# Optimization experiments

Hardware: AMD Instinct MI355X
Metric: run time of the kernel (lower is better)

Reference implementation:

```python
import jax, jax.numpy as jnp
import numpy as np
from jax import lax

# ---- static config (from init_kwargs / input_specs) ----
B, NB, C, F = 16, 8192, 3, 64   # batches, points-per-batch, coord dim, feat dim
RATIO, K = 0.125, 16
M = int(RATIO * NB)


def setup_inputs() -> dict:
    key = jax.random.key(0)
    kx, kp = jax.random.split(key)
    x = jax.random.normal(kx, (B * NB, F), dtype=jnp.float32)
    pos = jax.random.normal(kp, (B * NB, C), dtype=jnp.float32)
    batch = (jnp.arange(B * NB, dtype=jnp.int32) // NB).astype(jnp.int32)
    return {"x": x, "pos": pos, "batch": batch}


def _fps_single(pos_b):
    """Sequential farthest point sampling on (NB, C), deterministic start at 0.
    Returns (M,) int32 indices into pos_b."""
    n = pos_b.shape[0]

    def step(carry, _):
        min_d2, last = carry
        d2 = jnp.sum((pos_b - pos_b[last]) ** 2, axis=-1)   # (NB,)
        min_d2 = jnp.minimum(min_d2, d2)
        nxt = jnp.argmax(min_d2).astype(jnp.int32)
        return (min_d2, nxt), last

    init = (jnp.full((n,), jnp.finfo(pos_b.dtype).max, dtype=pos_b.dtype),
            jnp.int32(0))
    _, idx = lax.scan(step, init, None, length=M)
    return idx  # (M,)


def reference(x, pos, batch):
    # batch ids are block-constant (batch[i] = i // NB), so per-batch views are
    # simple reshapes -- same semantics as torch_cluster's batched fps/knn.
    pos_b = pos.reshape(B, NB, C)

    # --- farthest point sampling per batch ---
    fps_idx = jax.vmap(_fps_single)(pos_b)                            # (B, M)
    centroids = jnp.take_along_axis(pos_b, fps_idx[..., None], axis=1)  # (B, M, C)

    # --- k-NN: squared distances centroids -> all points of same batch ---
    d2 = (jnp.sum(centroids ** 2, axis=-1)[..., None]
          - 2.0 * jnp.einsum('bmc,bnc->bmn', centroids, pos_b)
          + jnp.sum(pos_b ** 2, axis=-1)[:, None, :])                 # (B, M, NB)
    _, nn_idx = lax.top_k(-d2, K)                                     # (B, M, K)

    # gather neighbor coordinates (== pos[groups_idx[1]])
    groups = jax.vmap(lambda p, i: p[i])(pos_b, nn_idx.reshape(B, M * K))  # (B, M*K, C)

    return centroids.reshape(B * M, C), groups.reshape(B * M * K, C)
```

## Files before the change

kernel.cpp:

```cpp
#include <hip/hip_runtime.h>
#include <float.h>
#include <math.h>

#define B_   16
#define NB_  8192
#define M_   1024
#define K_   16


typedef float v2f __attribute__((ext_vector_type(2)));

#define FPS_T 256
#define PPT   32
#define NPAIR (PPT/2)
#define NWAVE (FPS_T/64)

__global__ __launch_bounds__(FPS_T, 1) void fps_kernel(const float* __restrict__ pos,
                                                       float* __restrict__ cent)
{
    #pragma clang fp contract(off)
    const int b = blockIdx.x;
    const int t = threadIdx.x;
    const float* pb = pos + (size_t)b * NB_ * 3;
    float* cb = cent + (size_t)b * M_ * 3;

    __shared__ float4 spts[NB_];
    __shared__ unsigned long long wkey[2][NWAVE];

    for (int p = t; p < NB_; p += FPS_T) {
        const float* s = pb + (size_t)p * 3;
        spts[p] = make_float4(s[0], s[1], s[2], 0.0f);
    }

    v2f px2[NPAIR], py2[NPAIR], pz2[NPAIR], md2[NPAIR];
    #pragma unroll
    for (int jj = 0; jj < NPAIR; ++jj) {
        const float* s0 = pb + (size_t)(t*PPT + 2*jj) * 3;
        px2[jj] = (v2f){s0[0], s0[3]};
        py2[jj] = (v2f){s0[1], s0[4]};
        pz2[jj] = (v2f){s0[2], s0[5]};
        md2[jj] = (v2f){FLT_MAX, FLT_MAX};
    }
    __syncthreads();

    float lx = pb[0], ly = pb[1], lz = pb[2];
    float c0x=0,c0y=0,c0z=0,c1x=0,c1y=0,c1z=0,c2x=0,c2y=0,c2z=0,c3x=0,c3y=0,c3z=0;

    for (int m = 0; m < M_; ++m) {
        if (t == (m >> 2)) {
            const int sl = m & 3;
            if      (sl == 0) { c0x=lx; c0y=ly; c0z=lz; }
            else if (sl == 1) { c1x=lx; c1y=ly; c1z=lz; }
            else if (sl == 2) { c2x=lx; c2y=ly; c2z=lz; }
            else              { c3x=lx; c3y=ly; c3z=lz; }
        }
        if (m == M_ - 1) break;

        const v2f lxv = {lx,lx}, lyv = {ly,ly}, lzv = {lz,lz};
        v2f bmax2 = {-1.0f, -1.0f};
        #pragma unroll
        for (int jj = 0; jj < NPAIR; ++jj) {
            v2f dx = px2[jj] - lxv;
            v2f dy = py2[jj] - lyv;
            v2f dz = pz2[jj] - lzv;
            v2f d2 = (dx*dx + dy*dy) + dz*dz;
            v2f mj = __builtin_elementwise_min(md2[jj], d2);
            md2[jj] = mj;
            bmax2 = __builtin_elementwise_max(bmax2, mj);
        }
        float bm = fmaxf(bmax2.x, bmax2.y);

        float v = bm;
        {
            int vi;
            vi = __builtin_amdgcn_update_dpp(__float_as_int(v), __float_as_int(v), 0xB1,  0xF, 0xF, false);
            v = fmaxf(v, __int_as_float(vi));
            vi = __builtin_amdgcn_update_dpp(__float_as_int(v), __float_as_int(v), 0x4E,  0xF, 0xF, false);
            v = fmaxf(v, __int_as_float(vi));
            vi = __builtin_amdgcn_update_dpp(__float_as_int(v), __float_as_int(v), 0x141, 0xF, 0xF, false);
            v = fmaxf(v, __int_as_float(vi));
            vi = __builtin_amdgcn_update_dpp(__float_as_int(v), __float_as_int(v), 0x140, 0xF, 0xF, false);
            v = fmaxf(v, __int_as_float(vi));
            vi = __builtin_amdgcn_update_dpp(__float_as_int(v), __float_as_int(v), 0x142, 0xF, 0xF, false);
            v = fmaxf(v, __int_as_float(vi));
            vi = __builtin_amdgcn_update_dpp(__float_as_int(v), __float_as_int(v), 0x143, 0xF, 0xF, false);
            v = fmaxf(v, __int_as_float(vi));
        }
        const float wv = __int_as_float(__builtin_amdgcn_readlane(__float_as_int(v), 63));

        int jp = -1;
        #pragma unroll
        for (int jj = NPAIR - 1; jj >= 0; --jj) {
            if (md2[jj].y == wv) jp = 2*jj + 1;
            if (md2[jj].x == wv) jp = 2*jj;
        }
        const unsigned long long mk = __ballot(jp >= 0);
        const int wl = (int)__ffsll(mk) - 1;
        const int gi = __builtin_amdgcn_readlane(t*PPT + jp, wl);

        const int par = m & 1;
        if ((t & 63) == 0)
            wkey[par][t >> 6] = ((unsigned long long)__float_as_uint(wv) << 32) |
                                (unsigned int)(~gi);
        __syncthreads();

        unsigned long long kk = wkey[par][0];
        #pragma unroll
        for (int w = 1; w < NWAVE; ++w) {
            const unsigned long long e = wkey[par][w];
            kk = (e > kk) ? e : kk;
        }
        const int best = (int)(~(unsigned int)kk);

        const float4 c = spts[best];
        lx = c.x; ly = c.y; lz = c.z;
    }

    {
        float4* o = (float4*)(cb + (size_t)t * 12);
        o[0] = make_float4(c0x, c0y, c0z, c1x);
        o[1] = make_float4(c1y, c1z, c2x, c2y);
        o[2] = make_float4(c2z, c3x, c3y, c3z);
    }
}

#define KNN_T   256
#define CHUNK   1024
#define GRP     8
#define BCAP    16
#define BSTRIDE 17

__device__ __forceinline__ void topk_insert(float d2, int pi, float val[16], int idx[16])
{
    int r = 0;
    #pragma unroll
    for (int j = 0; j < 16; ++j) r += (val[j] <= d2) ? 1 : 0;
    #pragma unroll
    for (int j = 15; j >= 1; --j) {
        bool sh = (j > r);
        val[j] = sh ? val[j-1] : val[j];
        idx[j] = sh ? idx[j-1] : idx[j];
    }
    #pragma unroll
    for (int j = 0; j < 16; ++j) {
        bool pl = (j == r);
        val[j] = pl ? d2 : val[j];
        idx[j] = pl ? pi : idx[j];
    }
}

__global__ __launch_bounds__(KNN_T, 2) void knn_kernel(const float* __restrict__ pos,
    const float* __restrict__ cent, float* __restrict__ groups,
    unsigned long long* __restrict__ partials, int nsplit)
{
    #pragma clang fp contract(off)
    __shared__ float4 spts[CHUNK];
    __shared__ unsigned long long sbuf[KNN_T * BSTRIDE];

    const int wg = blockIdx.x;
    const int t  = threadIdx.x;
    const int per_b = 4 * nsplit;
    const int b  = wg / per_b;
    const int r  = wg % per_b;
    const int cg = r / nsplit;
    const int sp = r % nsplit;
    const int span  = NB_ / nsplit;
    const int pbase = sp * span;
    const int nchunks = span / CHUNK;

    const float* pb = pos + (size_t)b * NB_ * 3;
    const int mg = b * M_ + cg * KNN_T + t;
    const float cx = cent[(size_t)mg*3+0];
    const float cy = cent[(size_t)mg*3+1];
    const float cz = cent[(size_t)mg*3+2];
    const float cn2 = (cx*cx + cy*cy) + cz*cz;

    float val[16]; int idx[16];
    #pragma unroll
    for (int j = 0; j < 16; ++j) { val[j] = FLT_MAX; idx[j] = 0; }
    float tau = FLT_MAX;
    int cnt = 0;
    unsigned long long* mybuf = sbuf + t * BSTRIDE;

    for (int c = 0; c < nchunks; ++c) {
        const int ps = pbase + c * CHUNK;
        __syncthreads();
        for (int p = t; p < CHUNK; p += KNN_T) {
            const float* s = pb + (size_t)(ps + p) * 3;
            float x = s[0], y = s[1], z = s[2];
            float pn2 = (x*x + y*y) + z*z;
            spts[p] = make_float4(x, y, z, pn2);
        }
        __syncthreads();

        for (int p0 = 0; p0 < CHUNK; p0 += GRP) {
            if (__any(cnt > BCAP - GRP)) {
                int n = cnt; cnt = 0;
                for (int i = 0; i < n; ++i) {
                    unsigned long long e = mybuf[i];
                    float d = __uint_as_float((unsigned int)(e >> 32));
                    int pi  = (int)(e & 0xFFFFFFFFu);
                    if (d < val[15]) topk_insert(d, pi, val, idx);
                }
                tau = val[15];
            }
            float4 q[GRP];
            #pragma unroll
            for (int i = 0; i < GRP; ++i) q[i] = spts[p0 + i];
            float d2v[GRP];
            #pragma unroll
            for (int i = 0; i < GRP; ++i) {
                float dot = __builtin_fmaf(cz, q[i].z,
                            __builtin_fmaf(cy, q[i].y, cx * q[i].x));
                d2v[i] = (cn2 - 2.0f*dot) + q[i].w;
            }
            #pragma unroll
            for (int i = 0; i < GRP; ++i) {
                if (d2v[i] < tau) {
                    mybuf[cnt] = ((unsigned long long)__float_as_uint(d2v[i]) << 32) |
                                 (unsigned int)(ps + p0 + i);
                    ++cnt;
                }
            }
        }
    }
    {
        int n = cnt;
        for (int i = 0; i < n; ++i) {
            unsigned long long e = mybuf[i];
            float d = __uint_as_float((unsigned int)(e >> 32));
            int pi  = (int)(e & 0xFFFFFFFFu);
            if (d < val[15]) topk_insert(d, pi, val, idx);
        }
    }

    if (nsplit > 1) {
        unsigned long long* o = partials + ((size_t)mg * nsplit + sp) * 16;
        #pragma unroll
        for (int kq = 0; kq < 16; ++kq)
            o[kq] = ((unsigned long long)__float_as_uint(val[kq]) << 32) | (unsigned int)idx[kq];
    } else {
        float* g = groups + (size_t)mg * K_ * 3;
        #pragma unroll
        for (int kq = 0; kq < 16; ++kq) {
            const float* s = pb + (size_t)idx[kq] * 3;
            g[kq*3+0] = s[0]; g[kq*3+1] = s[1]; g[kq*3+2] = s[2];
        }
    }
}

__global__ __launch_bounds__(256, 2) void knn_merge(const float* __restrict__ pos,
    const unsigned long long* __restrict__ partials, float* __restrict__ groups,
    int nsplit)
{
    const int mg = blockIdx.x * 256 + threadIdx.x;
    const int b  = mg >> 10;
    const float* pb = pos + (size_t)b * NB_ * 3;

    float val[16]; int idx[16];
    #pragma unroll
    for (int j = 0; j < 16; ++j) { val[j] = FLT_MAX; idx[j] = 0; }
    for (int sp = 0; sp < nsplit; ++sp) {
        const unsigned long long* l = partials + ((size_t)mg * nsplit + sp) * 16;
        #pragma unroll
        for (int kq = 0; kq < 16; ++kq) {
            unsigned long long e = l[kq];
            float d = __uint_as_float((unsigned int)(e >> 32));
            int pi  = (int)(e & 0xFFFFFFFFu);
            if (d < val[15]) topk_insert(d, pi, val, idx);
        }
    }
    float* g = groups + (size_t)mg * K_ * 3;
    #pragma unroll
    for (int kq = 0; kq < 16; ++kq) {
        const float* s = pb + (size_t)idx[kq] * 3;
        g[kq*3+0] = s[0]; g[kq*3+1] = s[1]; g[kq*3+2] = s[2];
    }
}

extern "C" void kernel_launch(void* const* d_in, const int* in_sizes, int n_in,
                              void* d_out, int out_size, void* d_ws, size_t ws_size,
                              hipStream_t stream)
{
    (void)in_sizes; (void)n_in; (void)out_size;
    const float* pos = (const float*)d_in[1];
    float* out    = (float*)d_out;
    float* cent   = out;
    float* groups = out + (size_t)B_ * M_ * 3;

    fps_kernel<<<B_, FPS_T, 0, stream>>>(pos, cent);

    const size_t lst = (size_t)B_ * M_ * 16 * sizeof(unsigned long long);
    int nsplit = (ws_size >= 8*lst) ? 8 : (ws_size >= 4*lst) ? 4 : (ws_size >= 2*lst) ? 2 : 1;

    knn_kernel<<<B_ * 4 * nsplit, KNN_T, 0, stream>>>(pos, cent, groups,
                                                      (unsigned long long*)d_ws, nsplit);
    if (nsplit > 1)
        knn_merge<<<(B_ * M_) / 256, 256, 0, stream>>>(pos,
                                                      (const unsigned long long*)d_ws,
                                                      groups, nsplit);
}
```

Measured before the change: 1.209 ms.

## Fuse FPS and kNN into one persistent kernel with progress-flag overlap

```diff
diff --git a/kernel.cpp b/kernel.cpp
--- a/kernel.cpp
+++ b/kernel.cpp
@@ -14,6 +14,289 @@
 #define PPT   32
 #define NPAIR (PPT/2)
 #define NWAVE (FPS_T/64)
+
+#define KNN_T   256
+#define CHUNK   1024
+#define GRP     8
+#define BCAP    16
+#define BSTRIDE 17
+
+#define FPS_BLOCKS B_
+#define C012_WGS   (B_*3)
+#define SPLIT3     8
+
+__device__ __forceinline__ void topk_insert(float d2, int pi, float val[16], int idx[16])
+{
+    int r = 0;
+    #pragma unroll
+    for (int j = 0; j < 16; ++j) r += (val[j] <= d2) ? 1 : 0;
+    #pragma unroll
+    for (int j = 15; j >= 1; --j) {
+        bool sh = (j > r);
+        val[j] = sh ? val[j-1] : val[j];
+        idx[j] = sh ? idx[j-1] : idx[j];
+    }
+    #pragma unroll
+    for (int j = 0; j < 16; ++j) {
+        bool pl = (j == r);
+        val[j] = pl ? d2 : val[j];
+        idx[j] = pl ? pi : idx[j];
+    }
+}
+
+__global__ __launch_bounds__(256, 1) void fused_kernel(
+    const float* __restrict__ pos, float* __restrict__ cent,
+    float* __restrict__ groups, unsigned long long* __restrict__ partials,
+    unsigned int* __restrict__ progress, int split3)
+{
+    #pragma clang fp contract(off)
+    __shared__ float4 spts[NB_];
+    __shared__ unsigned long long wkey[2][NWAVE];
+
+    const int blk = blockIdx.x;
+    const int t   = threadIdx.x;
+
+    if (blk < FPS_BLOCKS) {
+        const int b = blk;
+        const float* pb = pos + (size_t)b * NB_ * 3;
+        float* cb = cent + (size_t)b * M_ * 3;
+
+        for (int p = t; p < NB_; p += FPS_T) {
+            const float* s = pb + (size_t)p * 3;
+            spts[p] = make_float4(s[0], s[1], s[2], 0.0f);
+        }
+
+        v2f px2[NPAIR], py2[NPAIR], pz2[NPAIR], md2[NPAIR];
+        #pragma unroll
+        for (int jj = 0; jj < NPAIR; ++jj) {
+            const float* s0 = pb + (size_t)(t*PPT + 2*jj) * 3;
+            px2[jj] = (v2f){s0[0], s0[3]};
+            py2[jj] = (v2f){s0[1], s0[4]};
+            pz2[jj] = (v2f){s0[2], s0[5]};
+            md2[jj] = (v2f){FLT_MAX, FLT_MAX};
+        }
+        __syncthreads();
+
+        float lx = pb[0], ly = pb[1], lz = pb[2];
+        float c0x=0,c0y=0,c0z=0,c1x=0,c1y=0,c1z=0,c2x=0,c2y=0,c2z=0,c3x=0,c3y=0,c3z=0;
+
+        for (int m = 0; m < M_; ++m) {
+            if (t == (m >> 2)) {
+                const int sl = m & 3;
+                if      (sl == 0) { c0x=lx; c0y=ly; c0z=lz; }
+                else if (sl == 1) { c1x=lx; c1y=ly; c1z=lz; }
+                else if (sl == 2) { c2x=lx; c2y=ly; c2z=lz; }
+                else              { c3x=lx; c3y=ly; c3z=lz; }
+            }
+
+            if ((m & 255) == 255) {
+                const int cg = m >> 8;
+                if ((t >> 6) == cg) {
+                    float4* o = (float4*)(cb + (size_t)t * 12);
+                    o[0] = make_float4(c0x, c0y, c0z, c1x);
+                    o[1] = make_float4(c1y, c1z, c2x, c2y);
+                    o[2] = make_float4(c2z, c3x, c3y, c3z);
+                    if ((t & 63) == 0)
+                        __hip_atomic_store(&progress[b], (unsigned)(cg + 1),
+                                           __ATOMIC_RELEASE, __HIP_MEMORY_SCOPE_AGENT);
+                }
+            }
+            if (m == M_ - 1) break;
+
+            const v2f lxv = {lx,lx}, lyv = {ly,ly}, lzv = {lz,lz};
+            v2f bmax2 = {-1.0f, -1.0f};
+            #pragma unroll
+            for (int jj = 0; jj < NPAIR; ++jj) {
+                v2f dx = px2[jj] - lxv;
+                v2f dy = py2[jj] - lyv;
+                v2f dz = pz2[jj] - lzv;
+                v2f d2 = (dx*dx + dy*dy) + dz*dz;
+                v2f mj = __builtin_elementwise_min(md2[jj], d2);
+                md2[jj] = mj;
+                bmax2 = __builtin_elementwise_max(bmax2, mj);
+            }
+            float bm = fmaxf(bmax2.x, bmax2.y);
+
+            float v = bm;
+            {
+                int vi;
+                vi = __builtin_amdgcn_update_dpp(__float_as_int(v), __float_as_int(v), 0xB1,  0xF, 0xF, false);
+                v = fmaxf(v, __int_as_float(vi));
+                vi = __builtin_amdgcn_update_dpp(__float_as_int(v), __float_as_int(v), 0x4E,  0xF, 0xF, false);
+                v = fmaxf(v, __int_as_float(vi));
+                vi = __builtin_amdgcn_update_dpp(__float_as_int(v), __float_as_int(v), 0x141, 0xF, 0xF, false);
+                v = fmaxf(v, __int_as_float(vi));
+                vi = __builtin_amdgcn_update_dpp(__float_as_int(v), __float_as_int(v), 0x140, 0xF, 0xF, false);
+                v = fmaxf(v, __int_as_float(vi));
+                vi = __builtin_amdgcn_update_dpp(__float_as_int(v), __float_as_int(v), 0x142, 0xF, 0xF, false);
+                v = fmaxf(v, __int_as_float(vi));
+                vi = __builtin_amdgcn_update_dpp(__float_as_int(v), __float_as_int(v), 0x143, 0xF, 0xF, false);
+                v = fmaxf(v, __int_as_float(vi));
+            }
+            const float wv = __int_as_float(__builtin_amdgcn_readlane(__float_as_int(v), 63));
+
+            int jp = -1;
+            #pragma unroll
+            for (int jj = NPAIR - 1; jj >= 0; --jj) {
+                if (md2[jj].y == wv) jp = 2*jj + 1;
+                if (md2[jj].x == wv) jp = 2*jj;
+            }
+            const unsigned long long mk = __ballot(jp >= 0);
+            const int wl = (int)__ffsll(mk) - 1;
+            const int gi = __builtin_amdgcn_readlane(t*PPT + jp, wl);
+
+            const int par = m & 1;
+            if ((t & 63) == 0)
+                wkey[par][t >> 6] = ((unsigned long long)__float_as_uint(wv) << 32) |
+                                    (unsigned int)(~gi);
+            __syncthreads();
+
+            unsigned long long kk = wkey[par][0];
+            #pragma unroll
+            for (int w = 1; w < NWAVE; ++w) {
+                const unsigned long long e = wkey[par][w];
+                kk = (e > kk) ? e : kk;
+            }
+            const int best = (int)(~(unsigned int)kk);
+
+            const float4 c = spts[best];
+            lx = c.x; ly = c.y; lz = c.z;
+        }
+        return;
+    }
+
+    const int r = blk - FPS_BLOCKS;
+    int b, cg, sp, span, pbase, direct;
+    if (r < C012_WGS) {
+        b = r / 3; cg = r % 3; sp = 0; span = NB_; pbase = 0; direct = 1;
+    } else {
+        const int r3 = r - C012_WGS;
+        cg = 3;
+        if (split3 == 1) { b = r3;      sp = 0;       span = NB_;        pbase = 0;        direct = 1; }
+        else             { b = r3 >> 3; sp = r3 & 7;  span = NB_/SPLIT3; pbase = sp*span;  direct = 0; }
+    }
+
+    if (t == 0) {
+        while (__hip_atomic_load(&progress[b], __ATOMIC_ACQUIRE,
+                                 __HIP_MEMORY_SCOPE_AGENT) < (unsigned)(cg + 1))
+            __builtin_amdgcn_s_sleep(64);
+    }
+    __syncthreads();
+
+    float4* kpts = spts;
+    unsigned long long* sbuf = (unsigned long long*)(spts + CHUNK);
+
+    const float* pb = pos + (size_t)b * NB_ * 3;
+    const int nchunks = span / CHUNK;
+    const int mg = b * M_ + cg * KNN_T + t;
+    const float cx = cent[(size_t)mg*3+0];
+    const float cy = cent[(size_t)mg*3+1];
+    const float cz = cent[(size_t)mg*3+2];
+    const float cn2 = (cx*cx + cy*cy) + cz*cz;
+
+    float val[16]; int idx[16];
+    #pragma unroll
+    for (int j = 0; j < 16; ++j) { val[j] = FLT_MAX; idx[j] = 0; }
+    float tau = FLT_MAX;
+    int cnt = 0;
+    unsigned long long* mybuf = sbuf + t * BSTRIDE;
+
+    for (int c = 0; c < nchunks; ++c) {
+        const int ps = pbase + c * CHUNK;
+        __syncthreads();
+        for (int p = t; p < CHUNK; p += KNN_T) {
+            const float* s = pb + (size_t)(ps + p) * 3;
+            float x = s[0], y = s[1], z = s[2];
+            float pn2 = (x*x + y*y) + z*z;
+            kpts[p] = make_float4(x, y, z, pn2);
+        }
+        __syncthreads();
+
+        for (int p0 = 0; p0 < CHUNK; p0 += GRP) {
+            if (__any(cnt > BCAP - GRP)) {
+                int n = cnt; cnt = 0;
+                for (int i = 0; i < n; ++i) {
+                    unsigned long long e = mybuf[i];
+                    float d = __uint_as_float((unsigned int)(e >> 32));
+                    int pi  = (int)(e & 0xFFFFFFFFu);
+                    if (d < val[15]) topk_insert(d, pi, val, idx);
+                }
+                tau = val[15];
+            }
+            float4 q[GRP];
+            #pragma unroll
+            for (int i = 0; i < GRP; ++i) q[i] = kpts[p0 + i];
+            float d2v[GRP];
+            #pragma unroll
+            for (int i = 0; i < GRP; ++i) {
+                float dot = __builtin_fmaf(cz, q[i].z,
+                            __builtin_fmaf(cy, q[i].y, cx * q[i].x));
+                d2v[i] = (cn2 - 2.0f*dot) + q[i].w;
+            }
+            #pragma unroll
+            for (int i = 0; i < GRP; ++i) {
+                if (d2v[i] < tau) {
+                    mybuf[cnt] = ((unsigned long long)__float_as_uint(d2v[i]) << 32) |
+                                 (unsigned int)(ps + p0 + i);
+                    ++cnt;
+                }
+            }
+        }
+    }
+    {
+        int n = cnt;
+        for (int i = 0; i < n; ++i) {
+            unsigned long long e = mybuf[i];
+            float d = __uint_as_float((unsigned int)(e >> 32));
+            int pi  = (int)(e & 0xFFFFFFFFu);
+            if (d < val[15]) topk_insert(d, pi, val, idx);
+        }
+    }
+
+    if (!direct) {
+        unsigned long long* o = partials + ((size_t)(b * 256 + t) * SPLIT3 + sp) * 16;
+        #pragma unroll
+        for (int kq = 0; kq < 16; ++kq)
+            o[kq] = ((unsigned long long)__float_as_uint(val[kq]) << 32) | (unsigned int)idx[kq];
+    } else {
+        float* g = groups + (size_t)mg * K_ * 3;
+        #pragma unroll
+        for (int kq = 0; kq < 16; ++kq) {
+            const float* s = pb + (size_t)idx[kq] * 3;
+            g[kq*3+0] = s[0]; g[kq*3+1] = s[1]; g[kq*3+2] = s[2];
+        }
+    }
+}
+
+__global__ __launch_bounds__(256, 2) void knn_merge3(const float* __restrict__ pos,
+    const unsigned long long* __restrict__ partials, float* __restrict__ groups)
+{
+    const int g  = blockIdx.x * 256 + threadIdx.x;
+    const int b  = g >> 8;
+    const int tt = g & 255;
+    const float* pb = pos + (size_t)b * NB_ * 3;
+
+    float val[16]; int idx[16];
+    #pragma unroll
+    for (int j = 0; j < 16; ++j) { val[j] = FLT_MAX; idx[j] = 0; }
+    for (int sp = 0; sp < SPLIT3; ++sp) {
+        const unsigned long long* l = partials + ((size_t)(b * 256 + tt) * SPLIT3 + sp) * 16;
+        #pragma unroll
+        for (int kq = 0; kq < 16; ++kq) {
+            unsigned long long e = l[kq];
+            float d = __uint_as_float((unsigned int)(e >> 32));
+            int pi  = (int)(e & 0xFFFFFFFFu);
+            if (d < val[15]) topk_insert(d, pi, val, idx);
+        }
+    }
+    const int mg = b * M_ + 3 * KNN_T + tt;
+    float* o = groups + (size_t)mg * K_ * 3;
+    #pragma unroll
+    for (int kq = 0; kq < 16; ++kq) {
+        const float* s = pb + (size_t)idx[kq] * 3;
+        o[kq*3+0] = s[0]; o[kq*3+1] = s[1]; o[kq*3+2] = s[2];
+    }
+}
 
 __global__ __launch_bounds__(FPS_T, 1) void fps_kernel(const float* __restrict__ pos,
                                                        float* __restrict__ cent)
@@ -124,37 +407,12 @@
     }
 }
 
-#define KNN_T   256
-#define CHUNK   1024
-#define GRP     8
-#define BCAP    16
-#define BSTRIDE 17
-
-__device__ __forceinline__ void topk_insert(float d2, int pi, float val[16], int idx[16])
-{
-    int r = 0;
-    #pragma unroll
-    for (int j = 0; j < 16; ++j) r += (val[j] <= d2) ? 1 : 0;
-    #pragma unroll
-    for (int j = 15; j >= 1; --j) {
-        bool sh = (j > r);
-        val[j] = sh ? val[j-1] : val[j];
-        idx[j] = sh ? idx[j-1] : idx[j];
-    }
-    #pragma unroll
-    for (int j = 0; j < 16; ++j) {
-        bool pl = (j == r);
-        val[j] = pl ? d2 : val[j];
-        idx[j] = pl ? pi : idx[j];
-    }
-}
-
 __global__ __launch_bounds__(KNN_T, 2) void knn_kernel(const float* __restrict__ pos,
     const float* __restrict__ cent, float* __restrict__ groups,
     unsigned long long* __restrict__ partials, int nsplit)
 {
     #pragma clang fp contract(off)
-    __shared__ float4 spts[CHUNK];
+    __shared__ float4 kpts[CHUNK];
     __shared__ unsigned long long sbuf[KNN_T * BSTRIDE];
 
     const int wg = blockIdx.x;
@@ -189,7 +447,7 @@
             const float* s = pb + (size_t)(ps + p) * 3;
             float x = s[0], y = s[1], z = s[2];
             float pn2 = (x*x + y*y) + z*z;
-            spts[p] = make_float4(x, y, z, pn2);
+            kpts[p] = make_float4(x, y, z, pn2);
         }
         __syncthreads();
 
@@ -206,7 +464,7 @@
             }
             float4 q[GRP];
             #pragma unroll
-            for (int i = 0; i < GRP; ++i) q[i] = spts[p0 + i];
+            for (int i = 0; i < GRP; ++i) q[i] = kpts[p0 + i];
             float d2v[GRP];
             #pragma unroll
             for (int i = 0; i < GRP; ++i) {
@@ -288,15 +546,32 @@
     float* cent   = out;
     float* groups = out + (size_t)B_ * M_ * 3;
 
-    fps_kernel<<<B_, FPS_T, 0, stream>>>(pos, cent);
-
-    const size_t lst = (size_t)B_ * M_ * 16 * sizeof(unsigned long long);
-    int nsplit = (ws_size >= 8*lst) ? 8 : (ws_size >= 4*lst) ? 4 : (ws_size >= 2*lst) ? 2 : 1;
-
-    knn_kernel<<<B_ * 4 * nsplit, KNN_T, 0, stream>>>(pos, cent, groups,
-                                                      (unsigned long long*)d_ws, nsplit);
-    if (nsplit > 1)
-        knn_merge<<<(B_ * M_) / 256, 256, 0, stream>>>(pos,
-                                                      (const unsigned long long*)d_ws,
-                                                      groups, nsplit);
-}
+    const size_t FLAGS = 256;
+    const size_t PART  = (size_t)B_ * 256 * SPLIT3 * 16 *
+                         sizeof(unsigned long long);
+
+    if (ws_size >= FLAGS) {
+        const int split3 = (ws_size >= FLAGS + PART) ? SPLIT3 : 1;
+        unsigned int* progress = (unsigned int*)d_ws;
+        unsigned long long* partials = (unsigned long long*)((char*)d_ws + FLAGS);
+
+        hipMemsetAsync(d_ws, 0, FLAGS, stream);
+
+        const int grid = FPS_BLOCKS + C012_WGS +
+                         (split3 == SPLIT3 ? B_ * SPLIT3 : B_);
+        fused_kernel<<<grid, 256, 0, stream>>>(pos, cent, groups, partials,
+                                               progress, split3);
+        if (split3 == SPLIT3)
+            knn_merge3<<<(B_ * 256) / 256, 256, 0, stream>>>(pos, partials, groups);
+    } else {
+        fps_kernel<<<B_, FPS_T, 0, stream>>>(pos, cent);
+        const size_t lst = (size_t)B_ * M_ * 16 * sizeof(unsigned long long);
+        int nsplit = (ws_size >= 8*lst) ? 8 : (ws_size >= 4*lst) ? 4 :
+                     (ws_size >= 2*lst) ? 2 : 1;
+        knn_kernel<<<B_ * 4 * nsplit, KNN_T, 0, stream>>>(pos, cent, groups,
+                                                          (unsigned long long*)d_ws, nsplit);
+        if (nsplit > 1)
+            knn_merge<<<(B_ * M_) / 256, 256, 0, stream>>>(pos,
+                (const unsigned long long*)d_ws, groups, nsplit);
+    }
+}
```

After: 1.446 ms. +19.7%, slower.
